# Kernel optimization log

Hardware: AMD Instinct MI355X
Metric: run time of the kernel (lower is better)

The kernel has to match this reference:

```python
import jax, jax.numpy as jnp
import numpy as np
import math

D_MODEL = 1024
D_K = 1024
D_V = 1024
B, S = 4, 2048


def setup_inputs() -> dict:
    key = jax.random.key(0)
    ks = jax.random.split(key, 6)
    scale = 1.0 / math.sqrt(D_MODEL)
    return {
        "q": jax.random.normal(ks[0], (B, S, D_MODEL), dtype=jnp.float32),
        "k": jax.random.normal(ks[1], (B, S, D_MODEL), dtype=jnp.float32),
        "v": jax.random.normal(ks[2], (B, S, D_MODEL), dtype=jnp.float32),
        "Wq": jax.random.normal(ks[3], (D_K, D_MODEL), dtype=jnp.float32) * scale,
        "bq": jnp.zeros((D_K,), dtype=jnp.float32),
        "Wk": jax.random.normal(ks[4], (D_K, D_MODEL), dtype=jnp.float32) * scale,
        "bk": jnp.zeros((D_K,), dtype=jnp.float32),
        "Wv": jax.random.normal(ks[5], (D_V, D_MODEL), dtype=jnp.float32) * scale,
        "bv": jnp.zeros((D_V,), dtype=jnp.float32),
    }


def reference(q, k, v, Wq, bq, Wk, bk, Wv, bv):
    # Linear projections (torch Linear: x @ W.T + b)
    qp = jnp.einsum("bsd,kd->bsk", q, Wq) + bq   # [B,S,d_k]
    kp = jnp.einsum("bsd,kd->bsk", k, Wk) + bk   # [B,S,d_k]
    vp = jnp.einsum("bsd,kd->bsk", v, Wv) + bv   # [B,S,d_v]
    # Scaled dot-product attention, full NxN score matrix as in source
    energies = jnp.einsum("bqk,bsk->bqs", qp, kp) / math.sqrt(D_K)  # [B,S,S]
    weights = jax.nn.softmax(energies, axis=-1)
    out = jnp.einsum("bqs,bsv->bqv", weights, vp)  # [B,S,d_v]
    return out
```

## Files before the change

kernel.cpp:

```cpp
#include <hip/hip_runtime.h>
#include <hip/hip_bf16.h>


typedef unsigned short u16;
typedef __attribute__((ext_vector_type(8))) short short8;
typedef __attribute__((ext_vector_type(4))) float f32x4;

typedef const __attribute__((address_space(1))) void* gptr_t;
typedef __attribute__((address_space(3))) void* sptr_t;

static __device__ __forceinline__ u16 f2bf(float f) {
    unsigned u = __float_as_uint(f);
    u += 0x7FFFu + ((u >> 16) & 1u);
    return (u16)(u >> 16);
}
static __device__ __forceinline__ float bf2f(u16 s) {
    return __uint_as_float(((unsigned)s) << 16);
}

static __device__ __forceinline__ void gll16(const u16* g, u16* l) {
    __builtin_amdgcn_global_load_lds((gptr_t)g, (sptr_t)l, 16, 0, 0);
}

__global__ __launch_bounds__(256) void cvt2(
    const float* __restrict__ a, u16* __restrict__ oa, long na,
    const float* __restrict__ b, u16* __restrict__ ob, long nb)
{
    const float* s = blockIdx.z ? b : a;
    u16* d = blockIdx.z ? ob : oa;
    const long n = blockIdx.z ? nb : na;
    const long stride = (long)gridDim.x * blockDim.x * 8;
    for (long i = ((long)blockIdx.x * blockDim.x + threadIdx.x) * 8; i < n; i += stride) {
        f32x4 x = *(const f32x4*)(s + i);
        f32x4 y = *(const f32x4*)(s + i + 4);
        short8 o;
#pragma unroll
        for (int j = 0; j < 4; ++j) { o[j] = (short)f2bf(x[j]); o[4 + j] = (short)f2bf(y[j]); }
        *(short8*)(d + i) = o;
    }
}

template <bool OUT_BF16, bool HAS_BIAS>
__global__ __launch_bounds__(256) void gemm_bt(
    const u16* __restrict__ A, const u16* __restrict__ B,
    const float* __restrict__ bias, void* __restrict__ Cv,
    int M, int N, int K, long sA, long sB, long sC, float scale)
{
    __shared__ __align__(16) u16 lA[4096], lB[4096];
    const int tid = threadIdx.x;
    const long bz = blockIdx.z;
    A += bz * sA;
    B += bz * sB;
    const int row0 = blockIdx.y * 128, col0 = blockIdx.x * 128;
    const int lane = tid & 63, wid = tid >> 6;

    const int srow = wid * 16 + (lane >> 2);
    const int scol = (lane & 3) * 8;
    const u16* ga = A + (long)(row0 + srow) * K + scol;
    const u16* gb = B + (long)(col0 + srow) * K + scol;
    const long g1 = 64L * K;
    u16* la0 = lA + wid * 512;
    u16* la1 = lA + 2048 + wid * 512;
    u16* lb0 = lB + wid * 512;
    u16* lb1 = lB + 2048 + wid * 512;

    const int wr = wid >> 1, wc = wid & 1;
    const int fq = lane >> 4, fr = lane & 15;
    const u16* pa[4];
    const u16* pb[4];
#pragma unroll
    for (int i = 0; i < 4; ++i) {
        pa[i] = lA + (wr * 64 + i * 16 + fr) * 32 + fq * 8;
        pb[i] = lB + (wc * 64 + i * 16 + fr) * 32 + fq * 8;
    }

    f32x4 acc[4][4] = {};
    const int KT = K >> 5;
    for (int kt = 0; kt < KT; ++kt) {
        const long ko = (long)kt * 32;
        gll16(ga + ko, la0);
        gll16(ga + ko + g1, la1);
        gll16(gb + ko, lb0);
        gll16(gb + ko + g1, lb1);
        __syncthreads();
        short8 af[4], bf[4];
#pragma unroll
        for (int i = 0; i < 4; ++i) af[i] = *(const short8*)pa[i];
#pragma unroll
        for (int i = 0; i < 4; ++i) bf[i] = *(const short8*)pb[i];
#pragma unroll
        for (int mi = 0; mi < 4; ++mi)
#pragma unroll
            for (int ni = 0; ni < 4; ++ni)
                acc[mi][ni] = __builtin_amdgcn_mfma_f32_16x16x32_bf16(
                    af[mi], bf[ni], acc[mi][ni], 0, 0, 0);
        __syncthreads();
    }

    float bcol[4];
#pragma unroll
    for (int ni = 0; ni < 4; ++ni)
        bcol[ni] = HAS_BIAS ? bias[col0 + wc * 64 + ni * 16 + fr] : 0.f;

#pragma unroll
    for (int mi = 0; mi < 4; ++mi) {
#pragma unroll
        for (int ni = 0; ni < 4; ++ni) {
            const int cc = col0 + wc * 64 + ni * 16 + fr;
#pragma unroll
            for (int j = 0; j < 4; ++j) {
                const int rr = row0 + wr * 64 + mi * 16 + fq * 4 + j;
                const float vv = acc[mi][ni][j] * scale + bcol[ni];
                if constexpr (OUT_BF16) {
                    ((u16*)Cv)[bz * sC + (long)rr * N + cc] = f2bf(vv);
                } else {
                    ((float*)Cv)[bz * sC + (long)rr * N + cc] = vv;
                }
            }
        }
    }
}

__global__ __launch_bounds__(256) void softmax_rows(u16* __restrict__ P, int S) {
    const long row = blockIdx.x;
    u16* p = P + row * (long)S;
    const int tid = threadIdx.x;
    const int wid = tid >> 6, lane = tid & 63;

    short8 v = *(const short8*)(p + tid * 8);
    float x[8];
#pragma unroll
    for (int j = 0; j < 8; ++j) x[j] = bf2f((u16)v[j]);

    float m = x[0];
#pragma unroll
    for (int j = 1; j < 8; ++j) m = fmaxf(m, x[j]);
#pragma unroll
    for (int off = 32; off > 0; off >>= 1) m = fmaxf(m, __shfl_xor(m, off));
    __shared__ float red[8];
    if (lane == 0) red[wid] = m;
    __syncthreads();
    m = fmaxf(fmaxf(red[0], red[1]), fmaxf(red[2], red[3]));

    float e[8], s = 0.f;
#pragma unroll
    for (int j = 0; j < 8; ++j) { e[j] = __expf(x[j] - m); s += e[j]; }
#pragma unroll
    for (int off = 32; off > 0; off >>= 1) s += __shfl_xor(s, off);
    if (lane == 0) red[4 + wid] = s;
    __syncthreads();
    s = red[4] + red[5] + red[6] + red[7];
    const float inv = 1.f / s;

    short8 o;
#pragma unroll
    for (int j = 0; j < 8; ++j) o[j] = (short)f2bf(e[j] * inv);
    *(short8*)(p + tid * 8) = o;
}

__global__ __launch_bounds__(256) void transpose_bf16(
    const u16* __restrict__ in, u16* __restrict__ out, int R, int C)
{
    __shared__ u16 t[64][72];
    const long z = blockIdx.z;
    in  += z * (long)R * C;
    out += z * (long)R * C;
    const int r0 = blockIdx.y * 64, c0 = blockIdx.x * 64;
    const int tid = threadIdx.x;

    const int r = tid >> 2, cc = (tid & 3) * 16;
    const short8* src = (const short8*)(in + (long)(r0 + r) * C + c0 + cc);
    short8 v0 = src[0], v1 = src[1];
#pragma unroll
    for (int j = 0; j < 8; ++j) {
        t[r][cc + j]     = (u16)v0[j];
        t[r][cc + 8 + j] = (u16)v1[j];
    }
    __syncthreads();

    const int c = tid >> 2, rr = (tid & 3) * 16;
    short8 o0, o1;
#pragma unroll
    for (int j = 0; j < 8; ++j) {
        o0[j] = (short)t[rr + j][c];
        o1[j] = (short)t[rr + 8 + j][c];
    }
    short8* dst = (short8*)(out + (long)(c0 + c) * R + r0 + rr);
    dst[0] = o0;
    dst[1] = o1;
}

extern "C" void kernel_launch(void* const* d_in, const int* in_sizes, int n_in,
                              void* d_out, int out_size, void* d_ws, size_t ws_size,
                              hipStream_t stream) {
    const float* q  = (const float*)d_in[0];
    const float* k  = (const float*)d_in[1];
    const float* v  = (const float*)d_in[2];
    const float* Wq = (const float*)d_in[3];
    const float* bq = (const float*)d_in[4];
    const float* Wk = (const float*)d_in[5];
    const float* bk = (const float*)d_in[6];
    const float* Wv = (const float*)d_in[7];
    const float* bv = (const float*)d_in[8];

    const int S = 2048, D = 1024;
    const long MiB = 1024L * 1024L;
    const long nQ = 4L * S * D;
    const long nW = (long)D * D;
    char* ws = (char*)d_ws;
    u16* sb  = (u16*)(ws + 0 * MiB);
    u16* wb  = (u16*)(ws + 16 * MiB);
    u16* qp  = (u16*)(ws + 18 * MiB);
    u16* kp  = (u16*)(ws + 34 * MiB);
    u16* vp  = (u16*)(ws + 50 * MiB);
    u16* P   = (u16*)(ws + 66 * MiB);
    u16* vpT = (u16*)(ws + 0 * MiB);

    dim3 blk(256);
    dim3 gproj(8, 64, 1);

    cvt2<<<dim3(512, 1, 2), blk, 0, stream>>>(q, sb, nQ, Wq, wb, nW);
    gemm_bt<true, true><<<gproj, blk, 0, stream>>>(sb, wb, bq, qp,
        8192, 1024, 1024, 0, 0, 0, 1.f);
    cvt2<<<dim3(512, 1, 2), blk, 0, stream>>>(k, sb, nQ, Wk, wb, nW);
    gemm_bt<true, true><<<gproj, blk, 0, stream>>>(sb, wb, bk, kp,
        8192, 1024, 1024, 0, 0, 0, 1.f);
    cvt2<<<dim3(512, 1, 2), blk, 0, stream>>>(v, sb, nQ, Wv, wb, nW);
    gemm_bt<true, true><<<gproj, blk, 0, stream>>>(sb, wb, bv, vp,
        8192, 1024, 1024, 0, 0, 0, 1.f);

    transpose_bf16<<<dim3(16, 32, 4), blk, 0, stream>>>(vp, vpT, S, D);

    gemm_bt<true, false><<<dim3(16, 16, 4), blk, 0, stream>>>(qp, kp, nullptr, P,
        2048, 2048, 1024, (long)S * D, (long)S * D, (long)S * S, 0.03125f);

    softmax_rows<<<dim3(4 * S), blk, 0, stream>>>(P, S);

    gemm_bt<false, false><<<dim3(8, 16, 4), blk, 0, stream>>>(P, vpT, nullptr,
        (float*)d_out, 2048, 1024, 2048, (long)S * S, (long)D * S, (long)S * D, 1.f);
}
```

Measured before the change: 390.5 us.

## Replace 128x128 GEMM with double-buffered 256x256 tile kernel using swizzled LDS

Replaces the simple 128x128 single-buffered GEMM with a 256x256-tile, 512-thread kernel. It uses 128 KB of dynamic LDS with double buffering, XOR-swizzled LDS layout to avoid bank conflicts, and interleaved global_load_lds prefetch with quadrant MFMA phases under explicit barriers and setprio. It also remaps workgroup IDs across XCDs for cache locality. The goal is more data reuse per tile and hiding of global-load latency, at the cost of fewer workgroups (e.g. 128 for projections) and high register/LDS pressure.

```diff
diff --git a/kernel.cpp b/kernel.cpp
--- a/kernel.cpp
+++ b/kernel.cpp
@@ -17,10 +17,14 @@
 static __device__ __forceinline__ float bf2f(u16 s) {
     return __uint_as_float(((unsigned)s) << 16);
 }
-
-static __device__ __forceinline__ void gll16(const u16* g, u16* l) {
+static __device__ __forceinline__ void gll16(const void* g, void* l) {
     __builtin_amdgcn_global_load_lds((gptr_t)g, (sptr_t)l, 16, 0, 0);
 }
+
+#define CFENCE asm volatile("" ::: "memory")
+#define SBAR do { CFENCE; __builtin_amdgcn_sched_barrier(0); \
+                  __builtin_amdgcn_s_barrier(); \
+                  __builtin_amdgcn_sched_barrier(0); CFENCE; } while (0)
 
 __global__ __launch_bounds__(256) void cvt2(
     const float* __restrict__ a, u16* __restrict__ oa, long na,
@@ -41,60 +45,108 @@
 }
 
 template <bool OUT_BF16, bool HAS_BIAS>
-__global__ __launch_bounds__(256) void gemm_bt(
+__global__ __launch_bounds__(512, 2) void gemm256(
     const u16* __restrict__ A, const u16* __restrict__ B,
     const float* __restrict__ bias, void* __restrict__ Cv,
-    int M, int N, int K, long sA, long sB, long sC, float scale)
+    int K, int lda, int ldb, int ldc, long sA, long sB, long sC, float scale)
 {
-    __shared__ __align__(16) u16 lA[4096], lB[4096];
+    extern __shared__ char lds[];
     const int tid = threadIdx.x;
-    const long bz = blockIdx.z;
+    const int lane = tid & 63, wid = tid >> 6;
+
+    const int gx = gridDim.x, gy = gridDim.y;
+    const int nwg = gx * gy * gridDim.z;
+    int bid = blockIdx.x + gx * (blockIdx.y + gy * blockIdx.z);
+    const int cpx = nwg >> 3;
+    bid = (bid & 7) * cpx + (bid >> 3);
+    const int bx = bid % gx;
+    const int rem = bid / gx;
+    const int by = rem % gy;
+    const long bz = rem / gy;
     A += bz * sA;
     B += bz * sB;
-    const int row0 = blockIdx.y * 128, col0 = blockIdx.x * 128;
-    const int lane = tid & 63, wid = tid >> 6;
-
-    const int srow = wid * 16 + (lane >> 2);
-    const int scol = (lane & 3) * 8;
-    const u16* ga = A + (long)(row0 + srow) * K + scol;
-    const u16* gb = B + (long)(col0 + srow) * K + scol;
-    const long g1 = 64L * K;
-    u16* la0 = lA + wid * 512;
-    u16* la1 = lA + 2048 + wid * 512;
-    u16* lb0 = lB + wid * 512;
-    u16* lb1 = lB + 2048 + wid * 512;
-
-    const int wr = wid >> 1, wc = wid & 1;
+    const int row0 = by * 256, col0 = bx * 256;
+
+    const int wr = wid >> 2, wc = wid & 3;
     const int fq = lane >> 4, fr = lane & 15;
-    const u16* pa[4];
-    const u16* pb[4];
-#pragma unroll
-    for (int i = 0; i < 4; ++i) {
-        pa[i] = lA + (wr * 64 + i * 16 + fr) * 32 + fq * 8;
-        pb[i] = lB + (wc * 64 + i * 16 + fr) * 32 + fq * 8;
-    }
-
-    f32x4 acc[4][4] = {};
-    const int KT = K >> 5;
-    for (int kt = 0; kt < KT; ++kt) {
-        const long ko = (long)kt * 32;
-        gll16(ga + ko, la0);
-        gll16(ga + ko + g1, la1);
-        gll16(gb + ko, lb0);
-        gll16(gb + ko + g1, lb1);
-        __syncthreads();
-        short8 af[4], bf[4];
-#pragma unroll
-        for (int i = 0; i < 4; ++i) af[i] = *(const short8*)pa[i];
-#pragma unroll
-        for (int i = 0; i < 4; ++i) bf[i] = *(const short8*)pb[i];
-#pragma unroll
-        for (int mi = 0; mi < 4; ++mi)
-#pragma unroll
-            for (int ni = 0; ni < 4; ++ni)
-                acc[mi][ni] = __builtin_amdgcn_mfma_f32_16x16x32_bf16(
-                    af[mi], bf[ni], acc[mi][ni], 0, 0, 0);
-        __syncthreads();
+
+    const int slot0 = ((fq) ^ (fr & 7)) << 4;
+    const int slot1 = ((4 + fq) ^ (fr & 7)) << 4;
+    const int aBase = (wr * 128 + fr) * 128;
+    const int bBase = 32768 + (wc * 64 + fr) * 128;
+
+    const int sgRow = lane >> 3;
+    const int sgColB = ((lane & 7) ^ sgRow) << 4;
+    const int asub = wid & 3;
+
+#define STAGE_A(T, Q) do { \
+    char* d_ = lds + (((T) & 1) << 16) + ((wr * 128 + (Q) * 64) * 128) + asub * 2048; \
+    const char* s_ = (const char*)(A + (long)(row0 + wr * 128 + (Q) * 64 + asub * 16 + sgRow) * lda + (T) * 64) + sgColB; \
+    gll16(s_, d_); \
+    gll16(s_ + (long)8 * lda * 2, d_ + 1024); \
+} while (0)
+#define STAGE_B(T, Q) do { \
+    char* d_ = lds + (((T) & 1) << 16) + 32768 + ((wc * 64 + (Q) * 32) * 128) + wr * 2048; \
+    const char* s_ = (const char*)(B + (long)(col0 + wc * 64 + (Q) * 32 + wr * 16 + sgRow) * ldb + (T) * 64) + sgColB; \
+    gll16(s_, d_); \
+    gll16(s_ + (long)8 * ldb * 2, d_ + 1024); \
+} while (0)
+
+#define RDA(MIBASE) do { \
+    const char* p_ = bufc + aBase + (MIBASE) * 2048; \
+    _Pragma("unroll") for (int mi_ = 0; mi_ < 4; ++mi_) { \
+        af[mi_ * 2 + 0] = *(const short8*)(p_ + mi_ * 2048 + slot0); \
+        af[mi_ * 2 + 1] = *(const short8*)(p_ + mi_ * 2048 + slot1); \
+    } \
+} while (0)
+#define RDB(NIBASE) do { \
+    const char* p_ = bufc + bBase + (NIBASE) * 2048; \
+    _Pragma("unroll") for (int ni_ = 0; ni_ < 2; ++ni_) { \
+        bf[ni_ * 2 + 0] = *(const short8*)(p_ + ni_ * 2048 + slot0); \
+        bf[ni_ * 2 + 1] = *(const short8*)(p_ + ni_ * 2048 + slot1); \
+    } \
+} while (0)
+
+#define QUAD(QM, QN) do { \
+    __builtin_amdgcn_s_setprio(1); \
+    _Pragma("unroll") for (int mi_ = 0; mi_ < 4; ++mi_) \
+    _Pragma("unroll") for (int ni_ = 0; ni_ < 2; ++ni_) { \
+        acc[(QM) * 4 + mi_][(QN) * 2 + ni_] = __builtin_amdgcn_mfma_f32_16x16x32_bf16( \
+            af[mi_ * 2 + 0], bf[ni_ * 2 + 0], acc[(QM) * 4 + mi_][(QN) * 2 + ni_], 0, 0, 0); \
+        acc[(QM) * 4 + mi_][(QN) * 2 + ni_] = __builtin_amdgcn_mfma_f32_16x16x32_bf16( \
+            af[mi_ * 2 + 1], bf[ni_ * 2 + 1], acc[(QM) * 4 + mi_][(QN) * 2 + ni_], 0, 0, 0); \
+    } \
+    __builtin_amdgcn_s_setprio(0); \
+} while (0)
+
+    f32x4 acc[8][4] = {};
+    short8 af[8], bf[4];
+    const int NT = K >> 6;
+
+    STAGE_A(0, 0); STAGE_A(0, 1); STAGE_B(0, 0); STAGE_B(0, 1);
+    if (NT > 1) {
+        STAGE_A(1, 0); STAGE_A(1, 1);
+        asm volatile("s_waitcnt vmcnt(4)" ::: "memory");
+    } else {
+        asm volatile("s_waitcnt vmcnt(0)" ::: "memory");
+    }
+    SBAR;
+
+    for (int t = 0; t < NT; ++t) {
+        const char* bufc = lds + ((t & 1) << 16);
+        RDA(0); RDB(0);
+        if (t + 1 < NT) { STAGE_B(t + 1, 0); STAGE_B(t + 1, 1); }
+        SBAR; QUAD(0, 0); SBAR;
+        RDB(2);
+        if (t + 2 < NT) STAGE_A(t + 2, 0);
+        SBAR; QUAD(0, 1); SBAR;
+        RDA(4);
+        SBAR; QUAD(1, 1); SBAR;
+        RDB(0);
+        if (t + 2 < NT) STAGE_A(t + 2, 1);
+        if (t < NT - 2) asm volatile("s_waitcnt vmcnt(4)" ::: "memory");
+        else            asm volatile("s_waitcnt vmcnt(0)" ::: "memory");
+        SBAR; QUAD(1, 0); SBAR;
     }
 
     float bcol[4];
@@ -103,22 +155,27 @@
         bcol[ni] = HAS_BIAS ? bias[col0 + wc * 64 + ni * 16 + fr] : 0.f;
 
 #pragma unroll
-    for (int mi = 0; mi < 4; ++mi) {
+    for (int mi = 0; mi < 8; ++mi) {
 #pragma unroll
         for (int ni = 0; ni < 4; ++ni) {
             const int cc = col0 + wc * 64 + ni * 16 + fr;
 #pragma unroll
             for (int j = 0; j < 4; ++j) {
-                const int rr = row0 + wr * 64 + mi * 16 + fq * 4 + j;
+                const int rr = row0 + wr * 128 + mi * 16 + fq * 4 + j;
                 const float vv = acc[mi][ni][j] * scale + bcol[ni];
                 if constexpr (OUT_BF16) {
-                    ((u16*)Cv)[bz * sC + (long)rr * N + cc] = f2bf(vv);
+                    ((u16*)Cv)[bz * sC + (long)rr * ldc + cc] = f2bf(vv);
                 } else {
-                    ((float*)Cv)[bz * sC + (long)rr * N + cc] = vv;
+                    ((float*)Cv)[bz * sC + (long)rr * ldc + cc] = vv;
                 }
             }
         }
     }
+#undef STAGE_A
+#undef STAGE_B
+#undef RDA
+#undef RDB
+#undef QUAD
 }
 
 __global__ __launch_bounds__(256) void softmax_rows(u16* __restrict__ P, int S) {
@@ -216,26 +273,34 @@
     u16* P   = (u16*)(ws + 66 * MiB);
     u16* vpT = (u16*)(ws + 0 * MiB);
 
-    dim3 blk(256);
-    dim3 gproj(8, 64, 1);
+    const int LDSB = 131072;
+    hipFuncSetAttribute(reinterpret_cast<const void*>(&gemm256<true, true>),
+                        hipFuncAttributeMaxDynamicSharedMemorySize, LDSB);
+    hipFuncSetAttribute(reinterpret_cast<const void*>(&gemm256<true, false>),
+                        hipFuncAttributeMaxDynamicSharedMemorySize, LDSB);
+    hipFuncSetAttribute(reinterpret_cast<const void*>(&gemm256<false, false>),
+                        hipFuncAttributeMaxDynamicSharedMemorySize, LDSB);
+
+    dim3 blk(256), gblk(512);
+    dim3 gproj(4, 32, 1);
 
     cvt2<<<dim3(512, 1, 2), blk, 0, stream>>>(q, sb, nQ, Wq, wb, nW);
-    gemm_bt<true, true><<<gproj, blk, 0, stream>>>(sb, wb, bq, qp,
-        8192, 1024, 1024, 0, 0, 0, 1.f);
+    gemm256<true, true><<<gproj, gblk, LDSB, stream>>>(sb, wb, bq, qp,
+        1024, 1024, 1024, 1024, 0, 0, 0, 1.f);
     cvt2<<<dim3(512, 1, 2), blk, 0, stream>>>(k, sb, nQ, Wk, wb, nW);
-    gemm_bt<true, true><<<gproj, blk, 0, stream>>>(sb, wb, bk, kp,
-        8192, 1024, 1024, 0, 0, 0, 1.f);
+    gemm256<true, true><<<gproj, gblk, LDSB, stream>>>(sb, wb, bk, kp,
+        1024, 1024, 1024, 1024, 0, 0, 0, 1.f);
     cvt2<<<dim3(512, 1, 2), blk, 0, stream>>>(v, sb, nQ, Wv, wb, nW);
-    gemm_bt<true, true><<<gproj, blk, 0, stream>>>(sb, wb, bv, vp,
-        8192, 1024, 1024, 0, 0, 0, 1.f);
+    gemm256<true, true><<<gproj, gblk, LDSB, stream>>>(sb, wb, bv, vp,
+        1024, 1024, 1024, 1024, 0, 0, 0, 1.f);
 
     transpose_bf16<<<dim3(16, 32, 4), blk, 0, stream>>>(vp, vpT, S, D);
 
-    gemm_bt<true, false><<<dim3(16, 16, 4), blk, 0, stream>>>(qp, kp, nullptr, P,
-        2048, 2048, 1024, (long)S * D, (long)S * D, (long)S * S, 0.03125f);
+    gemm256<true, false><<<dim3(8, 8, 4), gblk, LDSB, stream>>>(qp, kp, nullptr, P,
+        1024, 1024, 1024, 2048, (long)S * D, (long)S * D, (long)S * S, 0.03125f);
 
     softmax_rows<<<dim3(4 * S), blk, 0, stream>>>(P, S);
 
-    gemm_bt<false, false><<<dim3(8, 16, 4), blk, 0, stream>>>(P, vpT, nullptr,
-        (float*)d_out, 2048, 1024, 2048, (long)S * S, (long)D * S, (long)S * D, 1.f);
-}
+    gemm256<false, false><<<dim3(4, 8, 4), gblk, LDSB, stream>>>(P, vpT, nullptr,
+        (float*)d_out, 2048, 2048, 2048, 1024, (long)S * S, (long)D * S, (long)S * D, 1.f);
+}
```

New measurement: 369.7 us. -5.3%, faster.
